# Performance work log

Measured on AMD Instinct MI355X. Metric: run time of the kernel, lower is better.

Reference implementation:

```python
import jax, jax.numpy as jnp
import numpy as np

D = 128          # data_dim
H = 512          # hidden_dim
K = 10           # num_bins
BATCH = 32768
BOUND = 5.0
MINW = 1e-3
MINH = 1e-3
MIND = 1e-3
MASK = np.array([1.0] * (D // 2) + [0.0] * (D // 2), dtype=np.float32)
TIDX = np.where(MASK == 0)[0]  # transformed dims (static)


def _rqs_forward(x, uw, uh, ud):
    # x: [B, T]; uw/uh: [B, T, K]; ud: [B, T, K-1]
    w = jax.nn.softmax(uw, axis=-1)
    w = MINW + (1.0 - MINW * K) * w
    cw = jnp.pad(jnp.cumsum(w, axis=-1), ((0, 0), (0, 0), (1, 0)))
    cw = 2.0 * BOUND * cw - BOUND
    cw = cw.at[..., 0].set(-BOUND).at[..., -1].set(BOUND)
    w = cw[..., 1:] - cw[..., :-1]

    h = jax.nn.softmax(uh, axis=-1)
    h = MINH + (1.0 - MINH * K) * h
    ch = jnp.pad(jnp.cumsum(h, axis=-1), ((0, 0), (0, 0), (1, 0)))
    ch = 2.0 * BOUND * ch - BOUND
    ch = ch.at[..., 0].set(-BOUND).at[..., -1].set(BOUND)
    h = ch[..., 1:] - ch[..., :-1]

    d = MIND + jax.nn.softplus(ud)
    d = jnp.pad(d, ((0, 0), (0, 0), (1, 1)), constant_values=1.0)  # [B,T,K+1]

    inside = (x >= -BOUND) & (x <= BOUND)
    xc = jnp.clip(x, -BOUND, BOUND)  # avoid NaN for outside values

    # searchsorted(cw, x, right=True) - 1, clamped to [0, K-1]
    bin_idx = jnp.clip(jnp.sum(cw <= xc[..., None], axis=-1) - 1, 0, K - 1)

    def gat(a, idx):
        return jnp.take_along_axis(a, idx[..., None], axis=-1)[..., 0]

    wk = gat(w, bin_idx)
    cwk = gat(cw, bin_idx)
    hk = gat(h, bin_idx)
    chk = gat(ch, bin_idx)
    dk = gat(d, bin_idx)
    dk1 = gat(d, bin_idx + 1)

    theta = (xc - cwk) / wk
    s = hk / wk
    tm = theta * (1.0 - theta)
    den = s + (dk + dk1 - 2.0 * s) * tm
    num = hk * (s * theta * theta + dk * tm)
    y = chk + num / den
    ld = jnp.log(s * s * (dk1 * theta * theta + 2.0 * s * tm + dk * (1.0 - theta) ** 2)) - 2.0 * jnp.log(den)

    y = jnp.where(inside, y, x)
    ld = jnp.where(inside, ld, 0.0)
    return y, ld


def setup_inputs() -> dict:
    key = jax.random.key(0)
    ks = jax.random.split(key, 7)
    out_dim = D * (3 * K - 1)
    return {
        "z": jax.random.normal(ks[0], (BATCH, D), dtype=jnp.float32) * 2.0,
        "W1": jax.random.normal(ks[1], (H, D), dtype=jnp.float32) * 0.05,
        "b1": jnp.zeros((H,), dtype=jnp.float32),
        "W2": jax.random.normal(ks[2], (H, H), dtype=jnp.float32) * 0.05,
        "b2": jnp.zeros((H,), dtype=jnp.float32),
        "W3": jax.random.normal(ks[3], (out_dim, H), dtype=jnp.float32) * 0.05,
        "b3": jnp.zeros((out_dim,), dtype=jnp.float32),
    }


def reference(z, W1, b1, W2, b2, W3, b3):
    mask = jnp.asarray(MASK)
    z_a = z * mask
    hdn = jax.nn.relu(z_a @ W1.T + b1)
    hdn = jax.nn.relu(hdn @ W2.T + b2)
    p = (hdn @ W3.T + b3).reshape(-1, D, 3 * K - 1)
    uw, uh, ud = jnp.split(p, [K, 2 * K], axis=-1)

    zb = z[:, TIDX]
    xb, ld = _rqs_forward(zb, uw[:, TIDX], uh[:, TIDX], ud[:, TIDX])

    x = z.at[:, TIDX].set(xb)
    logdet = jnp.sum(ld, axis=1)
    x = jnp.where(jnp.isnan(x) | jnp.isinf(x), 0.0, x)
    logdet = jnp.where(jnp.isnan(logdet) | jnp.isinf(logdet), 0.0, logdet)
    return x, logdet
```

## Files before the change

kernel.cpp:

```cpp
#include <hip/hip_runtime.h>
#include <cmath>

#define BATCH 32768
#define DIM   128
#define HID   512
#define NPAD  2048

typedef __attribute__((ext_vector_type(8))) _Float16 half8;
typedef __attribute__((ext_vector_type(8))) short   short8v;
typedef __attribute__((ext_vector_type(4))) float   f32x4;
typedef unsigned short u16;


__device__ __forceinline__ u16 f2h(float f) {
  _Float16 h = (_Float16)f;
  union { _Float16 h; u16 u; } v; v.h = h; return v.u;
}

__device__ __forceinline__ void async16(const void* g, void* l) {
  __builtin_amdgcn_global_load_lds(
      (const __attribute__((address_space(1))) void*)g,
      (__attribute__((address_space(3))) void*)l, 16, 0, 0);
}

__device__ __forceinline__ void vwait(int n) {
  switch (n) {
    case 0:  asm volatile("s_waitcnt vmcnt(0)"  ::: "memory"); break;
    case 2:  asm volatile("s_waitcnt vmcnt(2)"  ::: "memory"); break;
    case 6:  asm volatile("s_waitcnt vmcnt(6)"  ::: "memory"); break;
    case 8:  asm volatile("s_waitcnt vmcnt(8)"  ::: "memory"); break;
    default: asm volatile("s_waitcnt vmcnt(12)" ::: "memory"); break;
  }
}

__device__ __forceinline__ int xcd_swz(int bid, int nwg) {
  int cpx = nwg >> 3;
  return (bid & 7) * cpx + (bid >> 3);
}


__global__ __launch_bounds__(256) void prep_all_v10(
    const float* __restrict__ z, const float* __restrict__ W1, const float* __restrict__ W2,
    const float* __restrict__ W3, const float* __restrict__ b3,
    u16* __restrict__ zh, u16* __restrict__ W1h, u16* __restrict__ W2h,
    u16* __restrict__ W3h, float* __restrict__ b3p) {
  const int bid = blockIdx.x;
  if (bid < 1024) {
    int id = bid * 256 + threadIdx.x;
    int l = id & 63, mb = (id >> 6) & 2047, kt = id >> 17;
    int r = mb * 16 + (l & 15);
    int k0 = kt * 32 + ((l >> 4) << 3);
    const float* src = z + (size_t)r * DIM + k0;
    short8v H;
#pragma unroll
    for (int j = 0; j < 8; ++j) H[j] = (short)f2h(src[j]);
    *(short8v*)(zh + (size_t)id * 8) = H;
  } else if (bid < 1168) {
    int id = (bid - 1024) * 256 + threadIdx.x;
    if (id < 4096) {
      int l = id & 63, mb = (id >> 6) & 31, kt = id >> 11;
      int r = mb * 16 + (l & 15);
      int k0 = kt * 32 + ((l >> 4) << 3);
      const float* src = W1 + (size_t)r * DIM + k0;
      short8v H;
#pragma unroll
      for (int j = 0; j < 8; ++j) H[j] = (short)f2h(src[j]);
      *(short8v*)(W1h + (size_t)id * 8) = H;
    } else {
      int id2 = id - 4096;
      int l = id2 & 63, mb = (id2 >> 6) & 31, kt = id2 >> 11;
      int r = mb * 16 + (l & 15);
      int k0 = kt * 32 + ((l >> 4) << 3);
      const float* src = W2 + (size_t)r * HID + k0;
      short8v H;
#pragma unroll
      for (int j = 0; j < 8; ++j) H[j] = (short)f2h(src[j]);
      *(short8v*)(W2h + (size_t)id2 * 8) = H;
    }
  } else if (bid < 1680) {
    int id = (bid - 1168) * 256 + threadIdx.x;
    int l = id & 63, mb = (id >> 6) & 127, kt = id >> 13;
    int n = mb * 16 + (l & 15);
    int k0 = kt * 32 + ((l >> 4) << 3);
    int g = n >> 5, kk = n & 31;
    short8v H;
    if (kk < 29) {
      const float* src = W3 + ((size_t)((g + 64) * 29 + kk)) * HID + k0;
#pragma unroll
      for (int j = 0; j < 8; ++j) H[j] = (short)f2h(src[j]);
    } else {
#pragma unroll
      for (int j = 0; j < 8; ++j) H[j] = 0;
    }
    *(short8v*)(W3h + (size_t)id * 8) = H;
  } else {
    int n = (bid - 1680) * 256 + threadIdx.x;
    int g = n >> 5, kk = n & 31;
    b3p[n] = (kk < 29) ? b3[(g + 64) * 29 + kk] : 0.f;
  }
}


__device__ __forceinline__ void stageA_v10(const u16* __restrict__ A, size_t ab, u16* Lb, int t) {
  async16(A + ab + t * 8,         Lb + t * 8);
  async16(A + ab + (t + 256) * 8, Lb + (t + 256) * 8);
}

template<int NKT>
__device__ __forceinline__ void gemm_mainloop_v10(
    const u16* __restrict__ A, const u16* __restrict__ B,
    int a_rb0, int a_rs16, int b_rb0, int b_rs16,
    u16* LDS, f32x4 acc[4][4]) {
  const int t = threadIdx.x;
  const int lane = t & 63;
  const int wv = t >> 6;
  const int wr = wv >> 1, wc = wv & 1;
  const size_t aStep = (size_t)a_rs16 * 512;
  const size_t bStep = (size_t)b_rs16 * 512;
  const size_t ab0 = (size_t)a_rb0 * 512;
  const u16* Bp = B + (((size_t)(b_rb0 + wc * 4)) * 64 + lane) * 8;

  half8 breg[3][4];
#pragma unroll
  for (int nf = 0; nf < 4; ++nf) breg[0][nf] = *(const half8*)(Bp + nf * 512);
  if (NKT > 1) {
#pragma unroll
    for (int nf = 0; nf < 4; ++nf) breg[1][nf] = *(const half8*)(Bp + bStep + nf * 512);
  }
  stageA_v10(A, ab0, LDS, t);
  if (NKT > 1) stageA_v10(A, ab0 + aStep, LDS + 4096, t);

#pragma unroll
  for (int kt = 0; kt < NKT; ++kt) {
    if (kt + 2 < NKT) {
#pragma unroll
      for (int nf = 0; nf < 4; ++nf)
        breg[(kt + 2) % 3][nf] = *(const half8*)(Bp + (size_t)(kt + 2) * bStep + nf * 512);
      stageA_v10(A, ab0 + (size_t)(kt + 2) * aStep, LDS + ((kt + 2) & 3) * 4096, t);
    }
    int n_after = (kt == 0) ? ((NKT > 1 ? 2 : 0) + (NKT > 2 ? 6 : 0))
                            : (((kt + 1 < NKT) ? 6 : 0) + ((kt + 2 < NKT) ? 6 : 0));
    vwait(n_after);
    __builtin_amdgcn_s_barrier();
    __builtin_amdgcn_sched_barrier(0);
    half8 a[4];
#pragma unroll
    for (int mf = 0; mf < 4; ++mf)
      a[mf] = *(const half8*)(LDS + (kt & 3) * 4096 + ((wr * 4 + mf) * 64 + lane) * 8);
#pragma unroll
    for (int mf = 0; mf < 4; ++mf)
#pragma unroll
      for (int nf = 0; nf < 4; ++nf)
        acc[mf][nf] = __builtin_amdgcn_mfma_f32_16x16x32_f16(a[mf], breg[kt % 3][nf], acc[mf][nf], 0, 0, 0);
  }
}


template<int NKT>
__global__ __launch_bounds__(256, 3) void gemm_relu_v10(
    const u16* __restrict__ A, const u16* __restrict__ B,
    const float* __restrict__ bias, u16* __restrict__ C, int a_rs16) {
  __shared__ __align__(16) u16 LDS[16384];
  const int bid = xcd_swz(blockIdx.x, gridDim.x);
  const int nt = bid & 3;
  const int mt = bid >> 2;
  const int m0 = mt << 7, n0 = nt << 7;
  f32x4 zero = {0.f, 0.f, 0.f, 0.f};
  f32x4 acc[4][4];
#pragma unroll
  for (int i = 0; i < 4; ++i)
#pragma unroll
    for (int j = 0; j < 4; ++j) acc[i][j] = zero;

  gemm_mainloop_v10<NKT>(A, B, m0 >> 4, a_rs16, n0 >> 4, 32, LDS, acc);

  const int lane = threadIdx.x & 63;
  const int wv = threadIdx.x >> 6;
  const int wr = wv >> 1, wc = wv & 1;
#pragma unroll
  for (int mf = 0; mf < 4; ++mf) {
#pragma unroll
    for (int nf = 0; nf < 4; ++nf) {
      int col = n0 + wc * 64 + nf * 16 + (lane & 15);
      float bv = bias[col];
#pragma unroll
      for (int r = 0; r < 4; ++r) {
        int row = m0 + wr * 64 + mf * 16 + (lane >> 4) * 4 + r;
        float v = fmaxf(acc[mf][nf][r] + bv, 0.f);
        int ktO = col >> 5, mbO = row >> 4;
        int lO = (row & 15) | (((col >> 3) & 3) << 4);
        int jO = col & 7;
        size_t off = (((size_t)ktO * (BATCH >> 4) + mbO) * 64 + lO) * 8 + jO;
        C[off] = f2h(v);
      }
    }
  }
}


__device__ __forceinline__ void rqs(float xin, const float uw[10], const float uh[10], const float ud9[9],
                                    float& yv, float& ldv) {
  float mw = uw[0];
#pragma unroll
  for (int i = 1; i < 10; ++i) mw = fmaxf(mw, uw[i]);
  float ew[10]; float sw = 0.f;
#pragma unroll
  for (int i = 0; i < 10; ++i) { ew[i] = __expf(uw[i] - mw); sw += ew[i]; }
  float invw = 0.99f / sw;
  float cw[11]; cw[0] = -5.f;
  {
    float run = 0.f;
#pragma unroll
    for (int i = 0; i < 10; ++i) { run += 0.001f + invw * ew[i]; cw[i + 1] = 10.f * run - 5.f; }
  }
  cw[10] = 5.f;
  float mh = uh[0];
#pragma unroll
  for (int i = 1; i < 10; ++i) mh = fmaxf(mh, uh[i]);
  float eh[10]; float sh = 0.f;
#pragma unroll
  for (int i = 0; i < 10; ++i) { eh[i] = __expf(uh[i] - mh); sh += eh[i]; }
  float invh = 0.99f / sh;
  float ch[11]; ch[0] = -5.f;
  {
    float run = 0.f;
#pragma unroll
    for (int i = 0; i < 10; ++i) { run += 0.001f + invh * eh[i]; ch[i + 1] = 10.f * run - 5.f; }
  }
  ch[10] = 5.f;
  float dv[11]; dv[0] = 1.f; dv[10] = 1.f;
#pragma unroll
  for (int i = 0; i < 9; ++i) {
    float x = ud9[i];
    float sp = fmaxf(x, 0.f) + __logf(1.f + __expf(-fabsf(x)));
    dv[i + 1] = 0.001f + sp;
  }

  float xc = fminf(fmaxf(xin, -5.f), 5.f);
  int b = 0;
#pragma unroll
  for (int j = 1; j <= 10; ++j) b += (cw[j] <= xc) ? 1 : 0;
  b = (b > 9) ? 9 : b;

  float wk = cw[1] - cw[0], cwk = cw[0], hk = ch[1] - ch[0], chk = ch[0], dk = dv[0], dk1 = dv[1];
#pragma unroll
  for (int j = 1; j < 10; ++j) {
    if (j == b) { wk = cw[j + 1] - cw[j]; cwk = cw[j]; hk = ch[j + 1] - ch[j]; chk = ch[j]; dk = dv[j]; dk1 = dv[j + 1]; }
  }

  float th = (xc - cwk) / wk;
  float sr = hk / wk;
  float omth = 1.f - th;
  float tm = th * omth;
  float den = sr + (dk + dk1 - 2.f * sr) * tm;
  float num = hk * (sr * th * th + dk * tm);
  float y = chk + num / den;
  float ld = __logf(sr * sr * (dk1 * th * th + 2.f * sr * tm + dk * omth * omth)) - 2.f * __logf(den);
  bool inside = (xin >= -5.f) && (xin <= 5.f);
  yv = inside ? y : xin;
  ldv = inside ? ld : 0.f;
  if (!isfinite(yv)) yv = 0.f;
}


__global__ __launch_bounds__(256, 3) void gemm3_spline_v10(
    const u16* __restrict__ A, const u16* __restrict__ B,
    const float* __restrict__ b3p, const float* __restrict__ z,
    float* __restrict__ xout, float* __restrict__ partial) {
  __shared__ __align__(16) char SMEM[33792];
  u16* LDS = (u16*)SMEM;
  float* PTf = (float*)SMEM;
  const int bid = xcd_swz(blockIdx.x, gridDim.x);
  const int nt = bid & 15;
  const int mt = bid >> 4;
  const int m0 = mt << 7, n0 = nt << 7;
  f32x4 zero = {0.f, 0.f, 0.f, 0.f};
  f32x4 acc[4][4];
#pragma unroll
  for (int i = 0; i < 4; ++i)
#pragma unroll
    for (int j = 0; j < 4; ++j) acc[i][j] = zero;

  gemm_mainloop_v10<16>(A, B, m0 >> 4, BATCH >> 4, n0 >> 4, NPAD >> 4, LDS, acc);

  const int t = threadIdx.x;
  const int lane = t & 63;
  const int wv = t >> 6;
  const int wr = wv >> 1, wc = wv & 1;
  const int gb = n0 >> 5;

  for (int p = 0; p < 2; ++p) {
    __syncthreads();
    if (wr == p) {
#pragma unroll
      for (int mf = 0; mf < 4; ++mf)
#pragma unroll
        for (int nf = 0; nf < 4; ++nf)
#pragma unroll
          for (int r = 0; r < 4; ++r) {
            int cl = wc * 64 + nf * 16 + (lane & 15);
            int rowl = mf * 16 + (lane >> 4) * 4 + r;
            PTf[rowl * 132 + (cl >> 5) * 33 + (cl & 31)] = acc[mf][nf][r];
          }
    }
    __syncthreads();

    const int rl = t >> 2;
    const int g = t & 3;
    const int row = p * 64 + rl;
    const int grow = m0 + row;
    const float* pr = PTf + rl * 132 + g * 33;
    const float* bb = b3p + n0 + g * 32;
    float uw[10], uh[10], ud9[9];
#pragma unroll
    for (int i = 0; i < 10; ++i) uw[i] = pr[i] + bb[i];
#pragma unroll
    for (int i = 0; i < 10; ++i) uh[i] = pr[10 + i] + bb[10 + i];
#pragma unroll
    for (int i = 0; i < 9; ++i) ud9[i] = pr[20 + i] + bb[20 + i];

    float xin = z[(long)grow * DIM + 64 + gb + g];
    float yv, ldv;
    rqs(xin, uw, uh, ud9, yv, ldv);

    xout[(long)grow * DIM + 64 + gb + g] = yv;

    float s = ldv;
    s += __shfl_down(s, 1);
    s += __shfl_down(s, 2);
    if (g == 0) partial[(long)nt * BATCH + grow] = s;
  }
}


__global__ __launch_bounds__(256) void copy_first_v10(const float* __restrict__ z, float* __restrict__ xout) {
  int id = blockIdx.x * 256 + threadIdx.x;
  int m = id >> 4, c4 = id & 15;
  const float4 v = *(const float4*)(z + (long)m * DIM + c4 * 4);
  *(float4*)(xout + (long)m * DIM + c4 * 4) = v;
}

__global__ __launch_bounds__(256) void reduce_ld_v10(const float* __restrict__ partial, float* __restrict__ ldout) {
  int row = blockIdx.x * 256 + threadIdx.x;
  float s = 0.f;
#pragma unroll
  for (int i = 0; i < 16; ++i) s += partial[(long)i * BATCH + row];
  if (!isfinite(s)) s = 0.f;
  ldout[row] = s;
}


extern "C" void kernel_launch(void* const* d_in, const int* in_sizes, int n_in,
                              void* d_out, int out_size, void* d_ws, size_t ws_size,
                              hipStream_t stream) {
  const float* z  = (const float*)d_in[0];
  const float* W1 = (const float*)d_in[1];
  const float* b1 = (const float*)d_in[2];
  const float* W2 = (const float*)d_in[3];
  const float* b2 = (const float*)d_in[4];
  const float* W3 = (const float*)d_in[5];
  const float* b3 = (const float*)d_in[6];
  float* xout  = (float*)d_out;
  float* ldout = xout + (size_t)BATCH * DIM;

  char* ws = (char*)d_ws;
  u16* W1h = (u16*)ws;  ws += (size_t)512 * 64 * 2;
  u16* W2h = (u16*)ws;  ws += (size_t)512 * 512 * 2;
  u16* W3h = (u16*)ws;  ws += (size_t)NPAD * HID * 2;
  float* b3p = (float*)ws; ws += (size_t)NPAD * 4;
  u16* zah  = (u16*)ws;
  float* part = (float*)ws; ws += (size_t)BATCH * 64 * 2;
  u16* h1h = (u16*)ws;  ws += (size_t)BATCH * HID * 2;
  u16* h2h = (u16*)ws;  ws += (size_t)BATCH * HID * 2;

  prep_all_v10<<<1688, 256, 0, stream>>>(z, W1, W2, W3, b3, zah, W1h, W2h, W3h, b3p);

  gemm_relu_v10<2><<<(BATCH / 128) * 4, 256, 0, stream>>>(zah, W1h, b1, h1h, BATCH >> 4);
  gemm_relu_v10<16><<<(BATCH / 128) * 4, 256, 0, stream>>>(h1h, W2h, b2, h2h, BATCH >> 4);
  gemm3_spline_v10<<<(BATCH / 128) * (NPAD / 128), 256, 0, stream>>>(h2h, W3h, b3p, z, xout, part);

  copy_first_v10<<<(BATCH * 16) / 256, 256, 0, stream>>>(z, xout);
  reduce_ld_v10<<<BATCH / 256, 256, 0, stream>>>(part, ldout);
}
```

Before: 149.5 us.

## Retile final GEMM+spline kernel to 256x256 tiles with 512 threads and LDS double-buffering

Rewrites the third GEMM fused with the spline epilogue to use 256x256 output tiles per workgroup with 8 waves. Both A and B are staged into LDS through async loads in a double-buffered, interleaved-phase schedule, and MFMA runs are wrapped in s_setprio. Larger tiles halve the global traffic per FLOP and the count of partial logdet slices (16 to 8), which trims the final reduce. The cost is 128KB of LDS and one workgroup per CU, which lowers occupancy and leaves latency hiding to the software pipeline.

```diff
diff --git a/kernel.cpp b/kernel.cpp
--- a/kernel.cpp
+++ b/kernel.cpp
@@ -23,7 +23,9 @@
       (__attribute__((address_space(3))) void*)l, 16, 0, 0);
 }
 
-__device__ __forceinline__ void vwait(int n) {
+__device__ __forceinline__ void vwait4()  { asm volatile("s_waitcnt vmcnt(4)" ::: "memory"); }
+__device__ __forceinline__ void vwait0()  { asm volatile("s_waitcnt vmcnt(0)" ::: "memory"); }
+__device__ __forceinline__ void vwaitN(int n) {
   switch (n) {
     case 0:  asm volatile("s_waitcnt vmcnt(0)"  ::: "memory"); break;
     case 2:  asm volatile("s_waitcnt vmcnt(2)"  ::: "memory"); break;
@@ -39,7 +41,7 @@
 }
 
 
-__global__ __launch_bounds__(256) void prep_all_v10(
+__global__ __launch_bounds__(256) void prep_all_v15(
     const float* __restrict__ z, const float* __restrict__ W1, const float* __restrict__ W2,
     const float* __restrict__ W3, const float* __restrict__ b3,
     u16* __restrict__ zh, u16* __restrict__ W1h, u16* __restrict__ W2h,
@@ -101,15 +103,15 @@
 }
 
 
-__device__ __forceinline__ void stageA_v10(const u16* __restrict__ A, size_t ab, u16* Lb, int t) {
+__device__ __forceinline__ void stageA_v15(const u16* __restrict__ A, size_t ab, u16* Lb, int t) {
   async16(A + ab + t * 8,         Lb + t * 8);
   async16(A + ab + (t + 256) * 8, Lb + (t + 256) * 8);
 }
 
 template<int NKT>
-__device__ __forceinline__ void gemm_mainloop_v10(
+__device__ __forceinline__ void gemm_mainloop_v15r(
     const u16* __restrict__ A, const u16* __restrict__ B,
-    int a_rb0, int a_rs16, int b_rb0, int b_rs16,
+    int a_mb0, int a_rs16, int b_nb0, int b_rs16,
     u16* LDS, f32x4 acc[4][4]) {
   const int t = threadIdx.x;
   const int lane = t & 63;
@@ -117,30 +119,30 @@
   const int wr = wv >> 1, wc = wv & 1;
   const size_t aStep = (size_t)a_rs16 * 512;
   const size_t bStep = (size_t)b_rs16 * 512;
-  const size_t ab0 = (size_t)a_rb0 * 512;
-  const u16* Bp = B + (((size_t)(b_rb0 + wc * 4)) * 64 + lane) * 8;
-
-  half8 breg[3][4];
-#pragma unroll
-  for (int nf = 0; nf < 4; ++nf) breg[0][nf] = *(const half8*)(Bp + nf * 512);
+  const size_t ab0 = (size_t)a_mb0 * 512;
+  const u16* Bp = B + (((size_t)(b_nb0 + wc * 4)) * 64 + lane) * 8;
+
+  half8 b[3][4];
+#pragma unroll
+  for (int nf = 0; nf < 4; ++nf) b[0][nf] = *(const half8*)(Bp + nf * 512);
   if (NKT > 1) {
 #pragma unroll
-    for (int nf = 0; nf < 4; ++nf) breg[1][nf] = *(const half8*)(Bp + bStep + nf * 512);
-  }
-  stageA_v10(A, ab0, LDS, t);
-  if (NKT > 1) stageA_v10(A, ab0 + aStep, LDS + 4096, t);
+    for (int nf = 0; nf < 4; ++nf) b[1][nf] = *(const half8*)(Bp + bStep + nf * 512);
+  }
+  stageA_v15(A, ab0, LDS, t);
+  if (NKT > 1) stageA_v15(A, ab0 + aStep, LDS + 4096, t);
 
 #pragma unroll
   for (int kt = 0; kt < NKT; ++kt) {
     if (kt + 2 < NKT) {
 #pragma unroll
       for (int nf = 0; nf < 4; ++nf)
-        breg[(kt + 2) % 3][nf] = *(const half8*)(Bp + (size_t)(kt + 2) * bStep + nf * 512);
-      stageA_v10(A, ab0 + (size_t)(kt + 2) * aStep, LDS + ((kt + 2) & 3) * 4096, t);
+        b[(kt + 2) % 3][nf] = *(const half8*)(Bp + (size_t)(kt + 2) * bStep + nf * 512);
+      stageA_v15(A, ab0 + (size_t)(kt + 2) * aStep, LDS + ((kt + 2) & 3) * 4096, t);
     }
     int n_after = (kt == 0) ? ((NKT > 1 ? 2 : 0) + (NKT > 2 ? 6 : 0))
                             : (((kt + 1 < NKT) ? 6 : 0) + ((kt + 2 < NKT) ? 6 : 0));
-    vwait(n_after);
+    vwaitN(n_after);
     __builtin_amdgcn_s_barrier();
     __builtin_amdgcn_sched_barrier(0);
     half8 a[4];
@@ -151,13 +153,12 @@
     for (int mf = 0; mf < 4; ++mf)
 #pragma unroll
       for (int nf = 0; nf < 4; ++nf)
-        acc[mf][nf] = __builtin_amdgcn_mfma_f32_16x16x32_f16(a[mf], breg[kt % 3][nf], acc[mf][nf], 0, 0, 0);
-  }
-}
-
+        acc[mf][nf] = __builtin_amdgcn_mfma_f32_16x16x32_f16(a[mf], b[kt % 3][nf], acc[mf][nf], 0, 0, 0);
+  }
+}
 
 template<int NKT>
-__global__ __launch_bounds__(256, 3) void gemm_relu_v10(
+__global__ __launch_bounds__(256, 3) void gemm_relu_v15(
     const u16* __restrict__ A, const u16* __restrict__ B,
     const float* __restrict__ bias, u16* __restrict__ C, int a_rs16) {
   __shared__ __align__(16) u16 LDS[16384];
@@ -172,7 +173,7 @@
 #pragma unroll
     for (int j = 0; j < 4; ++j) acc[i][j] = zero;
 
-  gemm_mainloop_v10<NKT>(A, B, m0 >> 4, a_rs16, n0 >> 4, 32, LDS, acc);
+  gemm_mainloop_v15r<NKT>(A, B, m0 >> 4, a_rs16, n0 >> 4, 32, LDS, acc);
 
   const int lane = threadIdx.x & 63;
   const int wv = threadIdx.x >> 6;
@@ -263,53 +264,127 @@
 }
 
 
-__global__ __launch_bounds__(256, 3) void gemm3_spline_v10(
+__global__ __launch_bounds__(512, 1) void gemm3_8ph_v15(
     const u16* __restrict__ A, const u16* __restrict__ B,
     const float* __restrict__ b3p, const float* __restrict__ z,
     float* __restrict__ xout, float* __restrict__ partial) {
-  __shared__ __align__(16) char SMEM[33792];
+  __shared__ __align__(16) char SMEM[131072];
   u16* LDS = (u16*)SMEM;
   float* PTf = (float*)SMEM;
   const int bid = xcd_swz(blockIdx.x, gridDim.x);
-  const int nt = bid & 15;
-  const int mt = bid >> 4;
-  const int m0 = mt << 7, n0 = nt << 7;
-  f32x4 zero = {0.f, 0.f, 0.f, 0.f};
-  f32x4 acc[4][4];
-#pragma unroll
-  for (int i = 0; i < 4; ++i)
-#pragma unroll
-    for (int j = 0; j < 4; ++j) acc[i][j] = zero;
-
-  gemm_mainloop_v10<16>(A, B, m0 >> 4, BATCH >> 4, n0 >> 4, NPAD >> 4, LDS, acc);
-
+  const int nt = bid & 7;
+  const int mt = bid >> 3;
+  const int m0 = mt << 8, n0 = nt << 8;
+  const int mb0 = m0 >> 4, nb0 = n0 >> 4;
   const int t = threadIdx.x;
   const int lane = t & 63;
-  const int wv = t >> 6;
-  const int wr = wv >> 1, wc = wv & 1;
-  const int gb = n0 >> 5;
-
-  for (int p = 0; p < 2; ++p) {
+  const int wid = t >> 6;
+  const int wr = wid >> 2;
+  const int wc = wid & 3;
+  constexpr int NITER = 8;
+  const size_t aStep = (size_t)(BATCH >> 4) * 512;
+  const size_t bStep = (size_t)(NPAD  >> 4) * 512;
+
+  f32x4 zero = {0.f, 0.f, 0.f, 0.f};
+  f32x4 acc[8][4];
+#pragma unroll
+  for (int i = 0; i < 8; ++i)
+#pragma unroll
+    for (int j = 0; j < 4; ++j) acc[i][j] = zero;
+
+#define STAGE_OP(p, kt0_, bufsel)                                                        \
+  {                                                                                      \
+    const int kt_ = (kt0_) + ((p) >> 2);                                                 \
+    const int h_ = (p) & 1;                                                              \
+    u16* dst_ = LDS + (bufsel) * 32768 + (p) * 4096 + t * 8;                             \
+    if (((p) & 2) == 0)                                                                  \
+      async16(B + ((size_t)kt_ * bStep) + (size_t)nb0 * 512 + h_ * 4096 + t * 8, dst_);  \
+    else                                                                                 \
+      async16(A + ((size_t)kt_ * aStep) + (size_t)mb0 * 512 + h_ * 4096 + t * 8, dst_);  \
+  }
+
+#pragma unroll
+  for (int p = 0; p < 8; ++p) STAGE_OP(p, 0, 0)
+
+#pragma unroll
+  for (int i = 0; i < NITER; ++i) {
+    u16* buf = LDS + (i & 1) * 32768;
+    const int b2 = (i + 1) & 1;
+    const bool more = (i + 1 < NITER);
+    const int ktn = 2 * (i + 1);
+
+    vwait4();
+    __builtin_amdgcn_s_barrier();
+    __builtin_amdgcn_sched_barrier(0);
+    {
+      half8 b0[4];
+#pragma unroll
+      for (int nf = 0; nf < 4; ++nf)
+        b0[nf] = *(const half8*)(buf + ((wc * 4 + nf) * 64 + lane) * 8);
+#pragma unroll
+      for (int q = 0; q < 4; ++q) {
+        half8 a0 = *(const half8*)(buf + 8192 + ((wr * 8 + 2 * q + 0) * 64 + lane) * 8);
+        half8 a1 = *(const half8*)(buf + 8192 + ((wr * 8 + 2 * q + 1) * 64 + lane) * 8);
+        if (more) { STAGE_OP(q, ktn, b2) }
+        __builtin_amdgcn_s_setprio(1);
+#pragma unroll
+        for (int nf = 0; nf < 4; ++nf) {
+          acc[2 * q + 0][nf] = __builtin_amdgcn_mfma_f32_16x16x32_f16(a0, b0[nf], acc[2 * q + 0][nf], 0, 0, 0);
+          acc[2 * q + 1][nf] = __builtin_amdgcn_mfma_f32_16x16x32_f16(a1, b0[nf], acc[2 * q + 1][nf], 0, 0, 0);
+        }
+        __builtin_amdgcn_s_setprio(0);
+      }
+    }
+
+    if (more) vwait4(); else vwait0();
+    __builtin_amdgcn_s_barrier();
+    __builtin_amdgcn_sched_barrier(0);
+    {
+      half8 b1[4];
+#pragma unroll
+      for (int nf = 0; nf < 4; ++nf)
+        b1[nf] = *(const half8*)(buf + 16384 + ((wc * 4 + nf) * 64 + lane) * 8);
+#pragma unroll
+      for (int q = 0; q < 4; ++q) {
+        half8 a0 = *(const half8*)(buf + 24576 + ((wr * 8 + 2 * q + 0) * 64 + lane) * 8);
+        half8 a1 = *(const half8*)(buf + 24576 + ((wr * 8 + 2 * q + 1) * 64 + lane) * 8);
+        if (more) { STAGE_OP(q + 4, ktn, b2) }
+        __builtin_amdgcn_s_setprio(1);
+#pragma unroll
+        for (int nf = 0; nf < 4; ++nf) {
+          acc[2 * q + 0][nf] = __builtin_amdgcn_mfma_f32_16x16x32_f16(a0, b1[nf], acc[2 * q + 0][nf], 0, 0, 0);
+          acc[2 * q + 1][nf] = __builtin_amdgcn_mfma_f32_16x16x32_f16(a1, b1[nf], acc[2 * q + 1][nf], 0, 0, 0);
+        }
+        __builtin_amdgcn_s_setprio(0);
+      }
+    }
+  }
+#undef STAGE_OP
+
+#pragma unroll
+  for (int s = 0; s < 4; ++s) {
     __syncthreads();
-    if (wr == p) {
-#pragma unroll
-      for (int mf = 0; mf < 4; ++mf)
+    if (wr == (s >> 1)) {
+#pragma unroll
+      for (int mfl = 0; mfl < 4; ++mfl) {
+        const int mf = (s & 1) * 4 + mfl;
 #pragma unroll
         for (int nf = 0; nf < 4; ++nf)
 #pragma unroll
           for (int r = 0; r < 4; ++r) {
-            int cl = wc * 64 + nf * 16 + (lane & 15);
-            int rowl = mf * 16 + (lane >> 4) * 4 + r;
-            PTf[rowl * 132 + (cl >> 5) * 33 + (cl & 31)] = acc[mf][nf][r];
+            int col = wc * 64 + nf * 16 + (lane & 15);
+            int rowl = mfl * 16 + (lane >> 4) * 4 + r;
+            PTf[rowl * 265 + (col >> 5) * 33 + (col & 31)] = acc[mf][nf][r];
           }
+      }
     }
     __syncthreads();
 
-    const int rl = t >> 2;
-    const int g = t & 3;
-    const int row = p * 64 + rl;
-    const int grow = m0 + row;
-    const float* pr = PTf + rl * 132 + g * 33;
+    const int row = t >> 3;
+    const int g = t & 7;
+    const int grow = m0 + s * 64 + row;
+    const int gdim = nt * 8 + g;
+    const float* pr = PTf + row * 265 + g * 33;
     const float* bb = b3p + n0 + g * 32;
     float uw[10], uh[10], ud9[9];
 #pragma unroll
@@ -319,32 +394,33 @@
 #pragma unroll
     for (int i = 0; i < 9; ++i) ud9[i] = pr[20 + i] + bb[20 + i];
 
-    float xin = z[(long)grow * DIM + 64 + gb + g];
+    float xin = z[(long)grow * DIM + 64 + gdim];
     float yv, ldv;
     rqs(xin, uw, uh, ud9, yv, ldv);
 
-    xout[(long)grow * DIM + 64 + gb + g] = yv;
-
-    float s = ldv;
-    s += __shfl_down(s, 1);
-    s += __shfl_down(s, 2);
-    if (g == 0) partial[(long)nt * BATCH + grow] = s;
-  }
-}
-
-
-__global__ __launch_bounds__(256) void copy_first_v10(const float* __restrict__ z, float* __restrict__ xout) {
+    xout[(long)grow * DIM + 64 + gdim] = yv;
+
+    float sld = ldv;
+    sld += __shfl_down(sld, 1);
+    sld += __shfl_down(sld, 2);
+    sld += __shfl_down(sld, 4);
+    if (g == 0) partial[(size_t)nt * BATCH + grow] = sld;
+  }
+}
+
+
+__global__ __launch_bounds__(256) void copy_first_v15(const float* __restrict__ z, float* __restrict__ xout) {
   int id = blockIdx.x * 256 + threadIdx.x;
   int m = id >> 4, c4 = id & 15;
   const float4 v = *(const float4*)(z + (long)m * DIM + c4 * 4);
   *(float4*)(xout + (long)m * DIM + c4 * 4) = v;
 }
 
-__global__ __launch_bounds__(256) void reduce_ld_v10(const float* __restrict__ partial, float* __restrict__ ldout) {
+__global__ __launch_bounds__(256) void reduce_ld_v15(const float* __restrict__ partial, float* __restrict__ ldout) {
   int row = blockIdx.x * 256 + threadIdx.x;
   float s = 0.f;
 #pragma unroll
-  for (int i = 0; i < 16; ++i) s += partial[(long)i * BATCH + row];
+  for (int i = 0; i < 8; ++i) s += partial[(long)i * BATCH + row];
   if (!isfinite(s)) s = 0.f;
   ldout[row] = s;
 }
@@ -373,12 +449,12 @@
   u16* h1h = (u16*)ws;  ws += (size_t)BATCH * HID * 2;
   u16* h2h = (u16*)ws;  ws += (size_t)BATCH * HID * 2;
 
-  prep_all_v10<<<1688, 256, 0, stream>>>(z, W1, W2, W3, b3, zah, W1h, W2h, W3h, b3p);
-
-  gemm_relu_v10<2><<<(BATCH / 128) * 4, 256, 0, stream>>>(zah, W1h, b1, h1h, BATCH >> 4);
-  gemm_relu_v10<16><<<(BATCH / 128) * 4, 256, 0, stream>>>(h1h, W2h, b2, h2h, BATCH >> 4);
-  gemm3_spline_v10<<<(BATCH / 128) * (NPAD / 128), 256, 0, stream>>>(h2h, W3h, b3p, z, xout, part);
-
-  copy_first_v10<<<(BATCH * 16) / 256, 256, 0, stream>>>(z, xout);
-  reduce_ld_v10<<<BATCH / 256, 256, 0, stream>>>(part, ldout);
-}
+  prep_all_v15<<<1688, 256, 0, stream>>>(z, W1, W2, W3, b3, zah, W1h, W2h, W3h, b3p);
+
+  gemm_relu_v15<2><<<(BATCH / 128) * 4, 256, 0, stream>>>(zah, W1h, b1, h1h, BATCH >> 4);
+  gemm_relu_v15<16><<<(BATCH / 128) * 4, 256, 0, stream>>>(h1h, W2h, b2, h2h, BATCH >> 4);
+  gemm3_8ph_v15<<<(BATCH / 256) * (NPAD / 256), 512, 0, stream>>>(h2h, W3h, b3p, z, xout, part);
+
+  copy_first_v15<<<(BATCH * 16) / 256, 256, 0, stream>>>(z, xout);
+  reduce_ld_v15<<<BATCH / 256, 256, 0, stream>>>(part, ldout);
+}
```

Measured after the change: 161.6 us. 8.1% more time.
